# Kernel tuning notes

Measured on AMD Instinct MI355X. Metric: run time of the kernel, lower is better.

Reference implementation:

```python
import jax, jax.numpy as jnp
import numpy as np

K = 1_000_000      # number of sparse (2D-det, 3D-anchor) candidate pairs
ROWS = 200         # max 2D detections
COLS = 70400       # number of 3D anchors (200*176*2)
SENTINEL = -9999999.0


def setup_inputs() -> dict:
    key = jax.random.key(0)
    ks = jax.random.split(key, 12)
    input_1 = jax.random.normal(ks[0], (1, 4, 1, K), dtype=jnp.float32)
    idx0 = jax.random.randint(ks[1], (K,), 0, ROWS)
    idx1 = jax.random.randint(ks[2], (K,), 0, COLS)
    tensor_index = jnp.stack([idx0, idx1], axis=1).astype(jnp.int64)
    # fuse_2d_3d: 1x1 Conv2d stack 4->18->36->36->1 (weights as (out,in) matrices)
    def w(k, o, i):
        return jax.random.normal(k, (o, i), dtype=jnp.float32) * (1.0 / np.sqrt(i))
    return {
        "input_1": input_1,
        "tensor_index": tensor_index,
        "W1": w(ks[3], 18, 4),  "b1": jnp.zeros((18,), jnp.float32),
        "W2": w(ks[4], 36, 18), "b2": jnp.zeros((36,), jnp.float32),
        "W3": w(ks[5], 36, 36), "b3": jnp.zeros((36,), jnp.float32),
        "W4": w(ks[6], 1, 36),  "b4": jnp.zeros((1,), jnp.float32),
    }


def reference(input_1, tensor_index, W1, b1, W2, b2, W3, b3, W4, b4):
    # 1x1 convs over (1,4,1,K) are channel matmuls over the K pair axis.
    x = input_1[0, :, 0, :]                                   # (4, K)
    h = jax.nn.relu(jnp.dot(W1, x) + b1[:, None])             # (18, K)
    h = jax.nn.relu(jnp.dot(W2, h) + b2[:, None])             # (36, K)
    h = jax.nn.relu(jnp.dot(W3, h) + b3[:, None])             # (36, K)
    v = (jnp.dot(W4, h) + b4[:, None])[0]                     # (K,) fused score per pair
    # Scatter into dense sentinel-filled grid, then max-reduce the 200 dim
    # (equivalent to MaxPool2d([200,1]) in the original).
    dense = jnp.full((ROWS, COLS), SENTINEL, dtype=input_1.dtype)
    dense = dense.at[tensor_index[:, 0], tensor_index[:, 1]].max(v)
    out = jnp.max(dense, axis=0).reshape(1, -1, 1)            # (1, 70400, 1)
    flag = 1
    return (out, flag)
```

## Files before the change

kernel.cpp:

```cpp
#include <hip/hip_runtime.h>

#define KN 1000000
#define NCOLS 70400
#define NPAIRS (KN / 32)
#define NBLK 1024
#define NTHR 256

typedef _Float16 f16x8 __attribute__((ext_vector_type(8)));
typedef float    f32x4 __attribute__((ext_vector_type(4)));

__device__ __forceinline__ unsigned encodeF(float f) {
    unsigned b = __float_as_uint(f);
    return (b & 0x80000000u) ? ~b : (b | 0x80000000u);
}
__device__ __forceinline__ float decodeF(unsigned e) {
    unsigned b = (e & 0x80000000u) ? (e & 0x7fffffffu) : ~e;
    return __uint_as_float(b);
}
#define ENC_SENT 0x34E76980u

#define MFMA16(a, b, c) __builtin_amdgcn_mfma_f32_16x16x32_f16((a), (b), (c), 0, 0, 0)

#define OW1 0
#define OB1 72
#define OW2 90
#define OB2 738
#define OW3 774
#define OB3 2070
#define OW4 2106
#define OB4 2142
#define NWTS 2143


__global__ __launch_bounds__(NTHR)
__attribute__((amdgpu_waves_per_eu(4, 4)))
void mlp_scatter_mfma(const float* __restrict__ x, const int* __restrict__ tidx,
                      const float* __restrict__ W1, const float* __restrict__ b1,
                      const float* __restrict__ W2, const float* __restrict__ b2,
                      const float* __restrict__ W3, const float* __restrict__ b3,
                      const float* __restrict__ W4, const float* __restrict__ b4,
                      unsigned* __restrict__ outU)
{
    __shared__ float    sw[NWTS];
    __shared__ _Float16 smem[4][2][1152];

    const int t    = threadIdx.x;
    const int lane = t & 63;
    const int wv   = t >> 6;
    const int quad = lane >> 4;
    const int n    = lane & 15;

    for (int i = t; i < 72;   i += NTHR) sw[OW1 + i] = W1[i];
    for (int i = t; i < 18;   i += NTHR) sw[OB1 + i] = b1[i];
    for (int i = t; i < 648;  i += NTHR) sw[OW2 + i] = W2[i];
    for (int i = t; i < 36;   i += NTHR) sw[OB2 + i] = b2[i];
    for (int i = t; i < 1296; i += NTHR) sw[OW3 + i] = W3[i];
    for (int i = t; i < 36;   i += NTHR) sw[OB3 + i] = b3[i];
    for (int i = t; i < 36;   i += NTHR) sw[OW4 + i] = W4[i];
    if (t == 0) sw[OB4] = b4[0];

    _Float16* Ha = &smem[wv][0][0];
    _Float16* Hb = &smem[wv][1][0];

    for (int i = lane; i < 128; i += 64) {
        const int row = i >> 3, dc = i & 7;
        ((unsigned*)(Ha + row * 72 + 48))[dc] = 0u;
        ((unsigned*)(Hb + row * 72 + 48))[dc] = 0u;
    }
    __syncthreads();

    auto bf = [&](int off, int OUT, int IN, int tt, int ks) {
        f16x8 r;
#pragma unroll
        for (int j = 0; j < 8; ++j) {
            int k  = ks * 32 + quad * 8 + j;
            int ng = tt * 16 + n;
            float w = (ng < OUT && k < IN) ? sw[off + ng * IN + k] : 0.0f;
            r[j] = (_Float16)w;
        }
        return r;
    };
    const f16x8 B1_0 = bf(OW1, 18,  4, 0, 0), B1_1 = bf(OW1, 18,  4, 1, 0);
    const f16x8 B2_0 = bf(OW2, 36, 18, 0, 0), B2_1 = bf(OW2, 36, 18, 1, 0), B2_2 = bf(OW2, 36, 18, 2, 0);
    const f16x8 B3_00 = bf(OW3, 36, 36, 0, 0), B3_01 = bf(OW3, 36, 36, 0, 1);
    const f16x8 B3_10 = bf(OW3, 36, 36, 1, 0), B3_11 = bf(OW3, 36, 36, 1, 1);
    const f16x8 B3_20 = bf(OW3, 36, 36, 2, 0), B3_21 = bf(OW3, 36, 36, 2, 1);

    const float bias1_0 = sw[OB1 + n];
    const float bias1_1 = (n < 2) ? sw[OB1 + 16 + n] : 0.0f;
    const float bias2_0 = sw[OB2 + n], bias2_1 = sw[OB2 + 16 + n];
    const float bias2_2 = (n < 4) ? sw[OB2 + 32 + n] : 0.0f;
    const float bias3_0 = sw[OB3 + n], bias3_1 = sw[OB3 + 16 + n];
    const float bias3_2 = (n < 4) ? sw[OB3 + 32 + n] : 0.0f;
    const float b4s = sw[OB4];
    const float w4_0 = sw[OW4 + n], w4_1 = sw[OW4 + 16 + n];
    const float w4_2 = (n < 4) ? sw[OW4 + 32 + n] : 0.0f;

    const int gw = (blockIdx.x * blockDim.x + t) >> 6;
    const int nw = (gridDim.x * blockDim.x) >> 6;

    float cxa0, cxa1, cxa2, cxa3, cxb0, cxb1, cxb2, cxb3;
    int cca = 0, ccb = 0;
    if (gw < NPAIRS) {
        const int kb = gw * 32;
        cxa0 = x[0 * KN + kb + n];      cxb0 = x[0 * KN + kb + 16 + n];
        cxa1 = x[1 * KN + kb + n];      cxb1 = x[1 * KN + kb + 16 + n];
        cxa2 = x[2 * KN + kb + n];      cxb2 = x[2 * KN + kb + 16 + n];
        cxa3 = x[3 * KN + kb + n];      cxb3 = x[3 * KN + kb + 16 + n];
        cca  = tidx[2 * (kb + n) + 1];  ccb  = tidx[2 * (kb + 16 + n) + 1];
    }

    for (int p = gw; p < NPAIRS; ) {
        const int pn = p + nw;
        const float xa0 = cxa0, xa1 = cxa1, xa2 = cxa2, xa3 = cxa3;
        const float xb0 = cxb0, xb1 = cxb1, xb2 = cxb2, xb3 = cxb3;
        const int cola = cca, colb = ccb;
        if (pn < NPAIRS) {
            const int kb = pn * 32;
            cxa0 = x[0 * KN + kb + n];      cxb0 = x[0 * KN + kb + 16 + n];
            cxa1 = x[1 * KN + kb + n];      cxb1 = x[1 * KN + kb + 16 + n];
            cxa2 = x[2 * KN + kb + n];      cxb2 = x[2 * KN + kb + 16 + n];
            cxa3 = x[3 * KN + kb + n];      cxb3 = x[3 * KN + kb + 16 + n];
            cca  = tidx[2 * (kb + n) + 1];  ccb  = tidx[2 * (kb + 16 + n) + 1];
        }

        f16x8 a1a = {}, a1b = {};
        if (quad == 0) {
            a1a[0] = (_Float16)xa0; a1a[1] = (_Float16)xa1;
            a1a[2] = (_Float16)xa2; a1a[3] = (_Float16)xa3;
            a1b[0] = (_Float16)xb0; a1b[1] = (_Float16)xb1;
            a1b[2] = (_Float16)xb2; a1b[3] = (_Float16)xb3;
        }
        f32x4 c0a = {bias1_0, bias1_0, bias1_0, bias1_0};
        f32x4 c1a = {bias1_1, bias1_1, bias1_1, bias1_1};
        f32x4 c0b = c0a, c1b = c1a;
        c0a = MFMA16(a1a, B1_0, c0a);  c0b = MFMA16(a1b, B1_0, c0b);
        c1a = MFMA16(a1a, B1_1, c1a);  c1b = MFMA16(a1b, B1_1, c1b);
#pragma unroll
        for (int r = 0; r < 4; ++r) {
            const int row = (quad * 4 + r) * 72;
            Ha[row + n]      = (_Float16)fmaxf(c0a[r], 0.0f);
            Ha[row + 16 + n] = (_Float16)fmaxf(c1a[r], 0.0f);
            Hb[row + n]      = (_Float16)fmaxf(c0b[r], 0.0f);
            Hb[row + 16 + n] = (_Float16)fmaxf(c1b[r], 0.0f);
        }

        const f16x8 a2a = *(const f16x8*)&Ha[n * 72 + quad * 8];
        const f16x8 a2b = *(const f16x8*)&Hb[n * 72 + quad * 8];
        f32x4 d0a = {bias2_0, bias2_0, bias2_0, bias2_0};
        f32x4 d1a = {bias2_1, bias2_1, bias2_1, bias2_1};
        f32x4 d2a = {bias2_2, bias2_2, bias2_2, bias2_2};
        f32x4 d0b = d0a, d1b = d1a, d2b = d2a;
        d0a = MFMA16(a2a, B2_0, d0a);  d0b = MFMA16(a2b, B2_0, d0b);
        d1a = MFMA16(a2a, B2_1, d1a);  d1b = MFMA16(a2b, B2_1, d1b);
        d2a = MFMA16(a2a, B2_2, d2a);  d2b = MFMA16(a2b, B2_2, d2b);
#pragma unroll
        for (int r = 0; r < 4; ++r) {
            const int row = (quad * 4 + r) * 72;
            Ha[row + n]      = (_Float16)fmaxf(d0a[r], 0.0f);
            Ha[row + 16 + n] = (_Float16)fmaxf(d1a[r], 0.0f);
            Ha[row + 32 + n] = (_Float16)fmaxf(d2a[r], 0.0f);
            Hb[row + n]      = (_Float16)fmaxf(d0b[r], 0.0f);
            Hb[row + 16 + n] = (_Float16)fmaxf(d1b[r], 0.0f);
            Hb[row + 32 + n] = (_Float16)fmaxf(d2b[r], 0.0f);
        }

        const f16x8 a30a = *(const f16x8*)&Ha[n * 72 + quad * 8];
        const f16x8 a31a = *(const f16x8*)&Ha[n * 72 + 32 + quad * 8];
        const f16x8 a30b = *(const f16x8*)&Hb[n * 72 + quad * 8];
        const f16x8 a31b = *(const f16x8*)&Hb[n * 72 + 32 + quad * 8];
        f32x4 e0a = {bias3_0, bias3_0, bias3_0, bias3_0};
        f32x4 e1a = {bias3_1, bias3_1, bias3_1, bias3_1};
        f32x4 e2a = {bias3_2, bias3_2, bias3_2, bias3_2};
        f32x4 e0b = e0a, e1b = e1a, e2b = e2a;
        e0a = MFMA16(a30a, B3_00, e0a);  e0a = MFMA16(a31a, B3_01, e0a);
        e1a = MFMA16(a30a, B3_10, e1a);  e1a = MFMA16(a31a, B3_11, e1a);
        e2a = MFMA16(a30a, B3_20, e2a);  e2a = MFMA16(a31a, B3_21, e2a);
        e0b = MFMA16(a30b, B3_00, e0b);  e0b = MFMA16(a31b, B3_01, e0b);
        e1b = MFMA16(a30b, B3_10, e1b);  e1b = MFMA16(a31b, B3_11, e1b);
        e2b = MFMA16(a30b, B3_20, e2b);  e2b = MFMA16(a31b, B3_21, e2b);

        float pa[4], pb[4];
#pragma unroll
        for (int r = 0; r < 4; ++r) {
            pa[r] = fmaf(w4_0, fmaxf(e0a[r], 0.0f),
                    fmaf(w4_1, fmaxf(e1a[r], 0.0f),
                         w4_2 * fmaxf(e2a[r], 0.0f)));
            pb[r] = fmaf(w4_0, fmaxf(e0b[r], 0.0f),
                    fmaf(w4_1, fmaxf(e1b[r], 0.0f),
                         w4_2 * fmaxf(e2b[r], 0.0f)));
        }
#pragma unroll
        for (int m = 8; m >= 1; m >>= 1) {
#pragma unroll
            for (int r = 0; r < 4; ++r) {
                pa[r] += __shfl_xor(pa[r], m, 16);
                pb[r] += __shfl_xor(pb[r], m, 16);
            }
        }
        if ((n >> 2) == quad) {
            const int r = n & 3;
            atomicMax(&outU[cola], encodeF(pa[r] + b4s) - ENC_SENT);
            atomicMax(&outU[colb], encodeF(pb[r] + b4s) - ENC_SENT);
        }

        p = pn;
    }
}

__global__ __launch_bounds__(256) void init_kernel(unsigned* __restrict__ outU) {
    int gid = blockIdx.x * blockDim.x + threadIdx.x;
    if (gid < NCOLS) outU[gid] = 0u;
}

__global__ __launch_bounds__(256) void decode_kernel(unsigned* __restrict__ outU,
                                                     int out_size) {
    int gid = blockIdx.x * blockDim.x + threadIdx.x;
    if (gid < out_size) {
        float r = (gid < NCOLS) ? decodeF(outU[gid] + ENC_SENT) : 1.0f;
        ((float*)outU)[gid] = r;
    }
}

extern "C" void kernel_launch(void* const* d_in, const int* in_sizes, int n_in,
                              void* d_out, int out_size, void* d_ws, size_t ws_size,
                              hipStream_t stream) {
    const float* x    = (const float*)d_in[0];
    const int*   tidx = (const int*)d_in[1];
    const float* W1 = (const float*)d_in[2];
    const float* b1 = (const float*)d_in[3];
    const float* W2 = (const float*)d_in[4];
    const float* b2 = (const float*)d_in[5];
    const float* W3 = (const float*)d_in[6];
    const float* b3 = (const float*)d_in[7];
    const float* W4 = (const float*)d_in[8];
    const float* b4 = (const float*)d_in[9];
    unsigned* outU = (unsigned*)d_out;

    init_kernel<<<(NCOLS + 255) / 256, 256, 0, stream>>>(outU);

    mlp_scatter_mfma<<<NBLK, NTHR, 0, stream>>>(
        x, tidx, W1, b1, W2, b2, W3, b3, W4, b4, outU);

    decode_kernel<<<(out_size + 255) / 256, 256, 0, stream>>>(outU, out_size);
}
```

Before: 133.7 us.

## Transpose MLP to weights-as-A MFMA layout, drop LDS staging for cross-lane permutes

Restructures the per-pair MLP so the weights become the MFMA A operand and the pairs sit on the N axis. Layer 1 is now computed with packed fp16 FMAs in registers instead of an MFMA. The shared-memory round trips between layers are replaced by ds_bpermute lane shuffles, and the final reduction becomes two xor-shuffles across quads. Occupancy is lowered from 4 to 3 waves per EU, which gives more registers but hides less latency. Computing layer 1 in fp16 may also reduce accuracy slightly.

Result: slower. 141.0 us (+5.5%).

```diff
diff --git a/kernel.cpp b/kernel.cpp
--- a/kernel.cpp
+++ b/kernel.cpp
@@ -7,7 +7,10 @@
 #define NTHR 256
 
 typedef _Float16 f16x8 __attribute__((ext_vector_type(8)));
+typedef _Float16 h2    __attribute__((ext_vector_type(2)));
 typedef float    f32x4 __attribute__((ext_vector_type(4)));
+typedef int      i32x4 __attribute__((ext_vector_type(4)));
+union F8 { f16x8 f; i32x4 i; };
 
 __device__ __forceinline__ unsigned encodeF(float f) {
     unsigned b = __float_as_uint(f);
@@ -20,6 +23,10 @@
 #define ENC_SENT 0x34E76980u
 
 #define MFMA16(a, b, c) __builtin_amdgcn_mfma_f32_16x16x32_f16((a), (b), (c), 0, 0, 0)
+
+__device__ __forceinline__ int h2i(h2 h) { int i; __builtin_memcpy(&i, &h, 4); return i; }
+__device__ __forceinline__ h2 hmax2z(h2 a) { return __builtin_elementwise_max(a, (h2)(_Float16)0); }
+__device__ __forceinline__ h2 pk(float lo, float hi) { return (h2){(_Float16)lo, (_Float16)hi}; }
 
 #define OW1 0
 #define OB1 72
@@ -33,7 +40,7 @@
 
 
 __global__ __launch_bounds__(NTHR)
-__attribute__((amdgpu_waves_per_eu(4, 4)))
+__attribute__((amdgpu_waves_per_eu(3, 3)))
 void mlp_scatter_mfma(const float* __restrict__ x, const int* __restrict__ tidx,
                       const float* __restrict__ W1, const float* __restrict__ b1,
                       const float* __restrict__ W2, const float* __restrict__ b2,
@@ -41,14 +48,12 @@
                       const float* __restrict__ W4, const float* __restrict__ b4,
                       unsigned* __restrict__ outU)
 {
-    __shared__ float    sw[NWTS];
-    __shared__ _Float16 smem[4][2][1152];
+    __shared__ float sw[NWTS];
 
     const int t    = threadIdx.x;
     const int lane = t & 63;
-    const int wv   = t >> 6;
-    const int quad = lane >> 4;
-    const int n    = lane & 15;
+    const int qd   = (lane >> 4) & 3;
+    const int e    = lane & 15;
 
     for (int i = t; i < 72;   i += NTHR) sw[OW1 + i] = W1[i];
     for (int i = t; i < 18;   i += NTHR) sw[OB1 + i] = b1[i];
@@ -58,56 +63,123 @@
     for (int i = t; i < 36;   i += NTHR) sw[OB3 + i] = b3[i];
     for (int i = t; i < 36;   i += NTHR) sw[OW4 + i] = W4[i];
     if (t == 0) sw[OB4] = b4[0];
-
-    _Float16* Ha = &smem[wv][0][0];
-    _Float16* Hb = &smem[wv][1][0];
-
-    for (int i = lane; i < 128; i += 64) {
-        const int row = i >> 3, dc = i & 7;
-        ((unsigned*)(Ha + row * 72 + 48))[dc] = 0u;
-        ((unsigned*)(Hb + row * 72 + 48))[dc] = 0u;
-    }
     __syncthreads();
 
-    auto bf = [&](int off, int OUT, int IN, int tt, int ks) {
-        f16x8 r;
+    h2 w1p[4][4], b1p[4];
+#pragma unroll
+    for (int j2 = 0; j2 < 4; ++j2) {
+        const int r0 = 8 * qd + 2 * j2, r1 = r0 + 1;
+#pragma unroll
+        for (int c = 0; c < 4; ++c) {
+            float fa = (r0 < 18) ? sw[OW1 + r0 * 4 + c] : 0.0f;
+            float fb = (r1 < 18) ? sw[OW1 + r1 * 4 + c] : 0.0f;
+            w1p[j2][c] = pk(fa, fb);
+        }
+        b1p[j2] = pk((r0 < 18) ? sw[OB1 + r0] : 0.0f,
+                     (r1 < 18) ? sw[OB1 + r1] : 0.0f);
+    }
+
+    auto af = [&](int off, int OUT, int IN, int T, int ks) {
+        F8 r;
 #pragma unroll
         for (int j = 0; j < 8; ++j) {
-            int k  = ks * 32 + quad * 8 + j;
-            int ng = tt * 16 + n;
-            float w = (ng < OUT && k < IN) ? sw[off + ng * IN + k] : 0.0f;
-            r[j] = (_Float16)w;
-        }
-        return r;
+            const int row = 16 * T + e, k = 32 * ks + 8 * qd + j;
+            r.f[j] = (_Float16)((row < OUT && k < IN) ? sw[off + row * IN + k] : 0.0f);
+        }
+        return r.f;
     };
-    const f16x8 B1_0 = bf(OW1, 18,  4, 0, 0), B1_1 = bf(OW1, 18,  4, 1, 0);
-    const f16x8 B2_0 = bf(OW2, 36, 18, 0, 0), B2_1 = bf(OW2, 36, 18, 1, 0), B2_2 = bf(OW2, 36, 18, 2, 0);
-    const f16x8 B3_00 = bf(OW3, 36, 36, 0, 0), B3_01 = bf(OW3, 36, 36, 0, 1);
-    const f16x8 B3_10 = bf(OW3, 36, 36, 1, 0), B3_11 = bf(OW3, 36, 36, 1, 1);
-    const f16x8 B3_20 = bf(OW3, 36, 36, 2, 0), B3_21 = bf(OW3, 36, 36, 2, 1);
-
-    const float bias1_0 = sw[OB1 + n];
-    const float bias1_1 = (n < 2) ? sw[OB1 + 16 + n] : 0.0f;
-    const float bias2_0 = sw[OB2 + n], bias2_1 = sw[OB2 + 16 + n];
-    const float bias2_2 = (n < 4) ? sw[OB2 + 32 + n] : 0.0f;
-    const float bias3_0 = sw[OB3 + n], bias3_1 = sw[OB3 + 16 + n];
-    const float bias3_2 = (n < 4) ? sw[OB3 + 32 + n] : 0.0f;
+    const f16x8 A2_0 = af(OW2, 36, 18, 0, 0), A2_1 = af(OW2, 36, 18, 1, 0), A2_2 = af(OW2, 36, 18, 2, 0);
+    const f16x8 A30_0 = af(OW3, 36, 36, 0, 0), A31_0 = af(OW3, 36, 36, 0, 1);
+    const f16x8 A30_1 = af(OW3, 36, 36, 1, 0), A31_1 = af(OW3, 36, 36, 1, 1);
+    const f16x8 A30_2 = af(OW3, 36, 36, 2, 0), A31_2 = af(OW3, 36, 36, 2, 1);
+
+    auto bvec = [&](int off, int T) {
+        f32x4 v;
+#pragma unroll
+        for (int r = 0; r < 4; ++r) {
+            const int m = 16 * T + 4 * qd + r;
+            v[r] = (m < 36) ? sw[off + m] : 0.0f;
+        }
+        return v;
+    };
+    const f32x4 B2V0 = bvec(OB2, 0), B2V1 = bvec(OB2, 1), B2V2 = bvec(OB2, 2);
+    const f32x4 B3V0 = bvec(OB3, 0), B3V1 = bvec(OB3, 1), B3V2 = bvec(OB3, 2);
+    const f32x4 W4V0 = bvec(OW4, 0), W4V1 = bvec(OW4, 1), W4V2 = bvec(OW4, 2);
     const float b4s = sw[OB4];
-    const float w4_0 = sw[OW4 + n], w4_1 = sw[OW4 + 16 + n];
-    const float w4_2 = (n < 4) ? sw[OW4 + 32 + n] : 0.0f;
+
+    const int idxA = ((((2 * qd) & 3) << 4) | e) << 2;
+    const int idxB = ((((2 * qd + 1) & 3) << 4) | e) << 2;
+    const int idxE = e << 2;
+    const bool lowT = (qd < 2);
+    const bool q0   = (qd == 0);
 
     const int gw = (blockIdx.x * blockDim.x + t) >> 6;
     const int nw = (gridDim.x * blockDim.x) >> 6;
+
+    auto tile = [&](float x0, float x1, float x2, float x3, int col) {
+        const h2 xp0 = pk(x0, x0), xp1 = pk(x1, x1);
+        const h2 xp2 = pk(x2, x2), xp3 = pk(x3, x3);
+        F8 b2f;
+#pragma unroll
+        for (int j2 = 0; j2 < 4; ++j2) {
+            h2 a = b1p[j2];
+            a = w1p[j2][0] * xp0 + a;
+            a = w1p[j2][1] * xp1 + a;
+            a = w1p[j2][2] * xp2 + a;
+            a = w1p[j2][3] * xp3 + a;
+            b2f.i[j2] = h2i(hmax2z(a));
+        }
+        const f32x4 D0 = MFMA16(A2_0, b2f.f, B2V0);
+        const f32x4 D1 = MFMA16(A2_1, b2f.f, B2V1);
+        const f32x4 D2 = MFMA16(A2_2, b2f.f, B2V2);
+        const int p01_0 = h2i(hmax2z(pk(D0[0], D0[1])));
+        const int p23_0 = h2i(hmax2z(pk(D0[2], D0[3])));
+        const int p01_1 = h2i(hmax2z(pk(D1[0], D1[1])));
+        const int p23_1 = h2i(hmax2z(pk(D1[2], D1[3])));
+        const int p01_2 = h2i(hmax2z(pk(D2[0], D2[1])));
+        const int p23_2 = h2i(hmax2z(pk(D2[2], D2[3])));
+        const int tA00 = __builtin_amdgcn_ds_bpermute(idxA, p01_0);
+        const int tA01 = __builtin_amdgcn_ds_bpermute(idxA, p01_1);
+        const int tA20 = __builtin_amdgcn_ds_bpermute(idxA, p23_0);
+        const int tA21 = __builtin_amdgcn_ds_bpermute(idxA, p23_1);
+        const int tB00 = __builtin_amdgcn_ds_bpermute(idxB, p01_0);
+        const int tB01 = __builtin_amdgcn_ds_bpermute(idxB, p01_1);
+        const int tB20 = __builtin_amdgcn_ds_bpermute(idxB, p23_0);
+        const int tB21 = __builtin_amdgcn_ds_bpermute(idxB, p23_1);
+        const int u0   = __builtin_amdgcn_ds_bpermute(idxE, p01_2);
+        const int u1   = __builtin_amdgcn_ds_bpermute(idxE, p23_2);
+        const int s0 = lowT ? tA00 : tA01;
+        const int s1 = lowT ? tA20 : tA21;
+        const int s2 = lowT ? tB00 : tB01;
+        const int s3 = lowT ? tB20 : tB21;
+        F8 b30, b31;
+        b30.i = (i32x4){s0, s1, s2, s3};
+        b31.i = (i32x4){q0 ? u0 : 0, q0 ? u1 : 0, 0, 0};
+        f32x4 E0 = MFMA16(A30_0, b30.f, B3V0); E0 = MFMA16(A31_0, b31.f, E0);
+        f32x4 E1 = MFMA16(A30_1, b30.f, B3V1); E1 = MFMA16(A31_1, b31.f, E1);
+        f32x4 E2 = MFMA16(A30_2, b30.f, B3V2); E2 = MFMA16(A31_2, b31.f, E2);
+        float v = 0.0f;
+#pragma unroll
+        for (int r = 0; r < 4; ++r) {
+            v = fmaf(W4V0[r], fmaxf(E0[r], 0.0f), v);
+            v = fmaf(W4V1[r], fmaxf(E1[r], 0.0f), v);
+            v = fmaf(W4V2[r], fmaxf(E2[r], 0.0f), v);
+        }
+        v += __shfl_xor(v, 16);
+        v += __shfl_xor(v, 32);
+        if (lane < 16) atomicMax(&outU[col], encodeF(v + b4s) - ENC_SENT);
+    };
 
     float cxa0, cxa1, cxa2, cxa3, cxb0, cxb1, cxb2, cxb3;
     int cca = 0, ccb = 0;
     if (gw < NPAIRS) {
         const int kb = gw * 32;
-        cxa0 = x[0 * KN + kb + n];      cxb0 = x[0 * KN + kb + 16 + n];
-        cxa1 = x[1 * KN + kb + n];      cxb1 = x[1 * KN + kb + 16 + n];
-        cxa2 = x[2 * KN + kb + n];      cxb2 = x[2 * KN + kb + 16 + n];
-        cxa3 = x[3 * KN + kb + n];      cxb3 = x[3 * KN + kb + 16 + n];
-        cca  = tidx[2 * (kb + n) + 1];  ccb  = tidx[2 * (kb + 16 + n) + 1];
+        cxa0 = x[0 * KN + kb + e];      cxb0 = x[0 * KN + kb + 16 + e];
+        cxa1 = x[1 * KN + kb + e];      cxb1 = x[1 * KN + kb + 16 + e];
+        cxa2 = x[2 * KN + kb + e];      cxb2 = x[2 * KN + kb + 16 + e];
+        cxa3 = x[3 * KN + kb + e];      cxb3 = x[3 * KN + kb + 16 + e];
+        cca  = ((const int2*)tidx)[kb + e].y;
+        ccb  = ((const int2*)tidx)[kb + 16 + e].y;
     }
 
     for (int p = gw; p < NPAIRS; ) {
@@ -117,93 +189,15 @@
         const int cola = cca, colb = ccb;
         if (pn < NPAIRS) {
             const int kb = pn * 32;
-            cxa0 = x[0 * KN + kb + n];      cxb0 = x[0 * KN + kb + 16 + n];
-            cxa1 = x[1 * KN + kb + n];      cxb1 = x[1 * KN + kb + 16 + n];
-            cxa2 = x[2 * KN + kb + n];      cxb2 = x[2 * KN + kb + 16 + n];
-            cxa3 = x[3 * KN + kb + n];      cxb3 = x[3 * KN + kb + 16 + n];
-            cca  = tidx[2 * (kb + n) + 1];  ccb  = tidx[2 * (kb + 16 + n) + 1];
-        }
-
-        f16x8 a1a = {}, a1b = {};
-        if (quad == 0) {
-            a1a[0] = (_Float16)xa0; a1a[1] = (_Float16)xa1;
-            a1a[2] = (_Float16)xa2; a1a[3] = (_Float16)xa3;
-            a1b[0] = (_Float16)xb0; a1b[1] = (_Float16)xb1;
-            a1b[2] = (_Float16)xb2; a1b[3] = (_Float16)xb3;
-        }
-        f32x4 c0a = {bias1_0, bias1_0, bias1_0, bias1_0};
-        f32x4 c1a = {bias1_1, bias1_1, bias1_1, bias1_1};
-        f32x4 c0b = c0a, c1b = c1a;
-        c0a = MFMA16(a1a, B1_0, c0a);  c0b = MFMA16(a1b, B1_0, c0b);
-        c1a = MFMA16(a1a, B1_1, c1a);  c1b = MFMA16(a1b, B1_1, c1b);
-#pragma unroll
-        for (int r = 0; r < 4; ++r) {
-            const int row = (quad * 4 + r) * 72;
-            Ha[row + n]      = (_Float16)fmaxf(c0a[r], 0.0f);
-            Ha[row + 16 + n] = (_Float16)fmaxf(c1a[r], 0.0f);
-            Hb[row + n]      = (_Float16)fmaxf(c0b[r], 0.0f);
-            Hb[row + 16 + n] = (_Float16)fmaxf(c1b[r], 0.0f);
-        }
-
-        const f16x8 a2a = *(const f16x8*)&Ha[n * 72 + quad * 8];
-        const f16x8 a2b = *(const f16x8*)&Hb[n * 72 + quad * 8];
-        f32x4 d0a = {bias2_0, bias2_0, bias2_0, bias2_0};
-        f32x4 d1a = {bias2_1, bias2_1, bias2_1, bias2_1};
-        f32x4 d2a = {bias2_2, bias2_2, bias2_2, bias2_2};
-        f32x4 d0b = d0a, d1b = d1a, d2b = d2a;
-        d0a = MFMA16(a2a, B2_0, d0a);  d0b = MFMA16(a2b, B2_0, d0b);
-        d1a = MFMA16(a2a, B2_1, d1a);  d1b = MFMA16(a2b, B2_1, d1b);
-        d2a = MFMA16(a2a, B2_2, d2a);  d2b = MFMA16(a2b, B2_2, d2b);
-#pragma unroll
-        for (int r = 0; r < 4; ++r) {
-            const int row = (quad * 4 + r) * 72;
-            Ha[row + n]      = (_Float16)fmaxf(d0a[r], 0.0f);
-            Ha[row + 16 + n] = (_Float16)fmaxf(d1a[r], 0.0f);
-            Ha[row + 32 + n] = (_Float16)fmaxf(d2a[r], 0.0f);
-            Hb[row + n]      = (_Float16)fmaxf(d0b[r], 0.0f);
-            Hb[row + 16 + n] = (_Float16)fmaxf(d1b[r], 0.0f);
-            Hb[row + 32 + n] = (_Float16)fmaxf(d2b[r], 0.0f);
-        }
-
-        const f16x8 a30a = *(const f16x8*)&Ha[n * 72 + quad * 8];
-        const f16x8 a31a = *(const f16x8*)&Ha[n * 72 + 32 + quad * 8];
-        const f16x8 a30b = *(const f16x8*)&Hb[n * 72 + quad * 8];
-        const f16x8 a31b = *(const f16x8*)&Hb[n * 72 + 32 + quad * 8];
-        f32x4 e0a = {bias3_0, bias3_0, bias3_0, bias3_0};
-        f32x4 e1a = {bias3_1, bias3_1, bias3_1, bias3_1};
-        f32x4 e2a = {bias3_2, bias3_2, bias3_2, bias3_2};
-        f32x4 e0b = e0a, e1b = e1a, e2b = e2a;
-        e0a = MFMA16(a30a, B3_00, e0a);  e0a = MFMA16(a31a, B3_01, e0a);
-        e1a = MFMA16(a30a, B3_10, e1a);  e1a = MFMA16(a31a, B3_11, e1a);
-        e2a = MFMA16(a30a, B3_20, e2a);  e2a = MFMA16(a31a, B3_21, e2a);
-        e0b = MFMA16(a30b, B3_00, e0b);  e0b = MFMA16(a31b, B3_01, e0b);
-        e1b = MFMA16(a30b, B3_10, e1b);  e1b = MFMA16(a31b, B3_11, e1b);
-        e2b = MFMA16(a30b, B3_20, e2b);  e2b = MFMA16(a31b, B3_21, e2b);
-
-        float pa[4], pb[4];
-#pragma unroll
-        for (int r = 0; r < 4; ++r) {
-            pa[r] = fmaf(w4_0, fmaxf(e0a[r], 0.0f),
-                    fmaf(w4_1, fmaxf(e1a[r], 0.0f),
-                         w4_2 * fmaxf(e2a[r], 0.0f)));
-            pb[r] = fmaf(w4_0, fmaxf(e0b[r], 0.0f),
-                    fmaf(w4_1, fmaxf(e1b[r], 0.0f),
-                         w4_2 * fmaxf(e2b[r], 0.0f)));
-        }
-#pragma unroll
-        for (int m = 8; m >= 1; m >>= 1) {
-#pragma unroll
-            for (int r = 0; r < 4; ++r) {
-                pa[r] += __shfl_xor(pa[r], m, 16);
-                pb[r] += __shfl_xor(pb[r], m, 16);
-            }
-        }
-        if ((n >> 2) == quad) {
-            const int r = n & 3;
-            atomicMax(&outU[cola], encodeF(pa[r] + b4s) - ENC_SENT);
-            atomicMax(&outU[colb], encodeF(pb[r] + b4s) - ENC_SENT);
-        }
-
+            cxa0 = x[0 * KN + kb + e];      cxb0 = x[0 * KN + kb + 16 + e];
+            cxa1 = x[1 * KN + kb + e];      cxb1 = x[1 * KN + kb + 16 + e];
+            cxa2 = x[2 * KN + kb + e];      cxb2 = x[2 * KN + kb + 16 + e];
+            cxa3 = x[3 * KN + kb + e];      cxb3 = x[3 * KN + kb + 16 + e];
+            cca  = ((const int2*)tidx)[kb + e].y;
+            ccb  = ((const int2*)tidx)[kb + 16 + e].y;
+        }
+        tile(xa0, xa1, xa2, xa3, cola);
+        tile(xb0, xb1, xb2, xb3, colb);
         p = pn;
     }
 }
```
